# Kernel optimization log

Hardware: AMD Instinct MI355X
Metric: run time of the kernel (lower is better)

## Reference

```python
import jax, jax.numpy as jnp
import numpy as np

N, D, H = 4096, 128, 8

def setup_inputs() -> dict:
    key = jax.random.key(0)
    ks = jax.random.split(key, 7)
    xavier = float(np.sqrt(6.0 / (D + D)))  # xavier_uniform for [*, D, D]
    x = jax.random.normal(ks[0], (N, D), dtype=jnp.float32)
    W_k = jax.random.uniform(ks[1], (H, D, D), minval=-xavier, maxval=xavier, dtype=jnp.float32)
    W_q = jax.random.uniform(ks[2], (H, D, D), minval=-xavier, maxval=xavier, dtype=jnp.float32)
    W_v = jax.random.uniform(ks[3], (H, D, D), minval=-xavier, maxval=xavier, dtype=jnp.float32)
    W_m = jnp.ones((H,), dtype=jnp.float32)
    lim = float(1.0 / np.sqrt(D))  # default torch Linear init range
    Wg = jax.random.uniform(ks[4], (D, D), minval=-lim, maxval=lim, dtype=jnp.float32)
    bg = jax.random.uniform(ks[5], (D,), minval=-lim, maxval=lim, dtype=jnp.float32)
    return {"x": x, "W_k": W_k, "W_q": W_q, "W_v": W_v, "W_m": W_m, "Wg": Wg, "bg": bg}

def reference(x, W_k, W_q, W_v, W_m, Wg, bg):
    # per-head projections: [H, N, D]
    q = jnp.einsum('nf,hfd->hnd', x, W_q)
    k = jnp.einsum('nf,hfd->hnd', x, W_k)
    v = jnp.einsum('nf,hfd->hnd', x, W_v)
    # dense all-pairs attention scores per head: [H, N, N]
    e = jnp.einsum('hnd,hmd->hnm', q, k)
    attn = jax.nn.softmax(e, axis=-1)
    # weighted sum over values, then head-scaled accumulation: [N, D]
    out = jnp.einsum('h,hnm,hmd->nd', W_m, attn, v)
    # residual MLP: x + ReLU(Linear(x + out))
    h = x + out
    g = jax.nn.relu(h @ Wg.T + bg)
    return x + g
```

## Files before the change

kernel.cpp:

```cpp
#include <hip/hip_runtime.h>

#define NROWS 4096
#define DDIM  128
#define NHEAD 8

typedef __attribute__((ext_vector_type(8))) short    short8;
typedef __attribute__((ext_vector_type(8))) _Float16 half8;
typedef __attribute__((ext_vector_type(4))) float    floatx4;

__device__ __forceinline__ float bf2f(unsigned short u){
  unsigned v = ((unsigned)u) << 16;
  return __builtin_bit_cast(float, v);
}
__device__ __forceinline__ unsigned short f2bf(float f){
  unsigned u = __builtin_bit_cast(unsigned, f);
  u += 0x7FFFu + ((u >> 16) & 1u);
  return (unsigned short)(u >> 16);
}
__device__ __forceinline__ void split2(float v, unsigned short& hi, unsigned short& lo){
  hi = f2bf(v);
  lo = f2bf(v - bf2f(hi));
}
__device__ __forceinline__ void async_cp16(const _Float16* g, _Float16* l){
  __builtin_amdgcn_global_load_lds(
      (const __attribute__((address_space(1))) void*)g,
      (__attribute__((address_space(3))) void*)l, 16, 0, 0);
}

__global__ void fill_kernel(float* __restrict__ out, float val, int n){
  int i = blockIdx.x * 256 + threadIdx.x;
  if (i < n) out[i] = val;
}

__global__ __launch_bounds__(256, 2) void proj_kernel(
    const float* __restrict__ x,
    const float* __restrict__ Wk, const float* __restrict__ Wv,
    _Float16* __restrict__ kfo, _Float16* __restrict__ vfo)
{
  __shared__ alignas(16) unsigned short wthi[DDIM][72];
  __shared__ alignas(16) unsigned short wtlo[DDIM][72];
  const int tid = threadIdx.x, lane = tid & 63, wave = tid >> 6;
  const int l4 = lane & 15, quad = lane >> 4;
  const int tile = blockIdx.x, h = blockIdx.y, z = blockIdx.z;
  const float* W = (z == 0 ? Wk : Wv) + h * DDIM * DDIM;

  floatx4 acc[8];
#pragma unroll
  for (int c = 0; c < 8; c++) acc[c] = (floatx4)0.f;

  for (int fh = 0; fh < 2; fh++) {
    for (int i = tid; i < DDIM * 64; i += 256) {
      const int d = i >> 6, fl = i & 63;
      unsigned short hi, lo;
      split2(W[(fh * 64 + fl) * DDIM + d], hi, lo);
      wthi[d][fl] = hi; wtlo[d][fl] = lo;
    }
    __syncthreads();

    const float* xr = x + (size_t)(tile * 64 + wave * 16 + l4) * DDIM + fh * 64 + quad * 8;
    short8 ah[2], al[2];
#pragma unroll
    for (int t2 = 0; t2 < 2; t2++) {
      float4 v0 = *(const float4*)(xr + t2 * 32);
      float4 v1 = *(const float4*)(xr + t2 * 32 + 4);
      float xv[8] = {v0.x, v0.y, v0.z, v0.w, v1.x, v1.y, v1.z, v1.w};
#pragma unroll
      for (int j = 0; j < 8; j++) {
        unsigned short hi, lo; split2(xv[j], hi, lo);
        ah[t2][j] = (short)hi; al[t2][j] = (short)lo;
      }
    }
#pragma unroll
    for (int t2 = 0; t2 < 2; t2++) {
#pragma unroll
      for (int c = 0; c < 8; c++) {
        short8 bh = *(const short8*)(&wthi[c * 16 + l4][t2 * 32 + quad * 8]);
        short8 bl = *(const short8*)(&wtlo[c * 16 + l4][t2 * 32 + quad * 8]);
        acc[c] = __builtin_amdgcn_mfma_f32_16x16x32_bf16(ah[t2], bh, acc[c], 0, 0, 0);
        acc[c] = __builtin_amdgcn_mfma_f32_16x16x32_bf16(al[t2], bh, acc[c], 0, 0, 0);
        acc[c] = __builtin_amdgcn_mfma_f32_16x16x32_bf16(ah[t2], bl, acc[c], 0, 0, 0);
      }
    }
    __syncthreads();
  }

  const int rb = wave * 16 + quad * 4;
  const size_t tilebase = (size_t)(h * 64 + tile) * 8192;
#pragma unroll
  for (int c = 0; c < 8; c++) {
    const int d = c * 16 + l4;
#pragma unroll
    for (int r = 0; r < 4; r++) {
      const int kl = rb + r;
      const float val = acc[c][r];
      if (z == 0) {
        const int c2 = kl >> 4, l4k = kl & 15;
        const int tt = d >> 5, qd = (d >> 3) & 3, jj = d & 7;
        const int qX = qd ^ ((l4k >> 1) & 3);
        kfo[tilebase + (size_t)((c2 * 4 + tt) * 16 + l4k) * 32 + qX * 8 + jj] =
            (_Float16)val;
      } else {
        const int c2 = d >> 4, l4v = d & 15;
        const int tt = kl >> 5, qd = (kl >> 3) & 3, jj = kl & 7;
        const int qX = qd ^ ((l4v >> 1) & 3);
        vfo[tilebase + (size_t)((c2 * 2 + tt) * 16 + l4v) * 32 + qX * 8 + jj] =
            (_Float16)val;
      }
    }
  }
}

union FlashLds {
  struct { unsigned short hi[DDIM][72], lo[DDIM][72]; } wq;
  float qf[64][132];
  struct { _Float16 k[8192], v[8192], p[4][2][1024]; } kv;
};

__global__ __launch_bounds__(256, 2) void flash_kernel(
    const float* __restrict__ x, const float* __restrict__ Wq,
    const _Float16* __restrict__ kfo, const _Float16* __restrict__ vfo,
    _Float16* __restrict__ op, float* __restrict__ mb, float* __restrict__ lb)
{
  __shared__ alignas(16) FlashLds lds;
  const int tid = threadIdx.x, lane = tid & 63, wave = tid >> 6;
  const int l4 = lane & 15, quad = lane >> 4;
  const int h = blockIdx.x & 7, qt = (blockIdx.x >> 3) & 31, s = blockIdx.x >> 8;
  const int q0 = qt * 128;

  half8 aq[2][4];

  {
    floatx4 qacc[2][8];
#pragma unroll
    for (int sp = 0; sp < 2; sp++)
#pragma unroll
      for (int c = 0; c < 8; c++) qacc[sp][c] = (floatx4)0.f;

    const float* Wqh = Wq + h * DDIM * DDIM;
    for (int fh = 0; fh < 2; fh++) {
      for (int i = tid; i < DDIM * 64; i += 256) {
        const int d = i >> 6, fl = i & 63;
        unsigned short hi, lo;
        split2(Wqh[(fh * 64 + fl) * DDIM + d], hi, lo);
        lds.wq.hi[d][fl] = hi; lds.wq.lo[d][fl] = lo;
      }
      __syncthreads();
#pragma unroll
      for (int sp = 0; sp < 2; sp++) {
        const float* xr = x + (size_t)(q0 + sp * 64 + wave * 16 + l4) * DDIM + fh * 64 + quad * 8;
        short8 ah[2], al[2];
#pragma unroll
        for (int t2 = 0; t2 < 2; t2++) {
          float4 v0 = *(const float4*)(xr + t2 * 32);
          float4 v1 = *(const float4*)(xr + t2 * 32 + 4);
          float xv[8] = {v0.x, v0.y, v0.z, v0.w, v1.x, v1.y, v1.z, v1.w};
#pragma unroll
          for (int j = 0; j < 8; j++) {
            unsigned short hi, lo; split2(xv[j], hi, lo);
            ah[t2][j] = (short)hi; al[t2][j] = (short)lo;
          }
        }
#pragma unroll
        for (int t2 = 0; t2 < 2; t2++) {
#pragma unroll
          for (int c = 0; c < 8; c++) {
            short8 bh = *(const short8*)(&lds.wq.hi[c * 16 + l4][t2 * 32 + quad * 8]);
            short8 bl = *(const short8*)(&lds.wq.lo[c * 16 + l4][t2 * 32 + quad * 8]);
            qacc[sp][c] = __builtin_amdgcn_mfma_f32_16x16x32_bf16(ah[t2], bh, qacc[sp][c], 0, 0, 0);
            qacc[sp][c] = __builtin_amdgcn_mfma_f32_16x16x32_bf16(al[t2], bh, qacc[sp][c], 0, 0, 0);
            qacc[sp][c] = __builtin_amdgcn_mfma_f32_16x16x32_bf16(ah[t2], bl, qacc[sp][c], 0, 0, 0);
          }
        }
      }
      __syncthreads();
    }

#pragma unroll
    for (int sp = 0; sp < 2; sp++) {
#pragma unroll
      for (int c = 0; c < 8; c++)
#pragma unroll
        for (int r = 0; r < 4; r++)
          lds.qf[wave * 16 + quad * 4 + r][c * 16 + l4] = qacc[sp][c][r];
      __syncthreads();
      if ((wave >> 1) == sp) {
#pragma unroll
        for (int g = 0; g < 2; g++)
#pragma unroll
          for (int t = 0; t < 4; t++) {
            const float* qr = &lds.qf[(wave & 1) * 32 + g * 16 + l4][t * 32 + quad * 8];
            float4 v0 = *(const float4*)qr;
            float4 v1 = *(const float4*)(qr + 4);
            aq[g][t][0] = (_Float16)v0.x; aq[g][t][1] = (_Float16)v0.y;
            aq[g][t][2] = (_Float16)v0.z; aq[g][t][3] = (_Float16)v0.w;
            aq[g][t][4] = (_Float16)v1.x; aq[g][t][5] = (_Float16)v1.y;
            aq[g][t][6] = (_Float16)v1.z; aq[g][t][7] = (_Float16)v1.w;
          }
      }
      __syncthreads();
    }
  }

  float m_run[2][4];
#pragma unroll
  for (int g = 0; g < 2; g++)
#pragma unroll
    for (int r = 0; r < 4; r++) m_run[g][r] = -1e30f;
  floatx4 Oacc[2][8], lacc[2];
#pragma unroll
  for (int g = 0; g < 2; g++) {
    lacc[g] = (floatx4)0.f;
#pragma unroll
    for (int c = 0; c < 8; c++) Oacc[g][c] = (floatx4)0.f;
  }

  half8 vones;
#pragma unroll
  for (int j = 0; j < 8; j++) vones[j] = (_Float16)1.f;

  const _Float16* kfo_h = kfo + (size_t)h * 64 * 8192;
  const _Float16* vfo_h = vfo + (size_t)h * 64 * 8192;
  const int lq = (l4 * 4 + (quad ^ ((l4 >> 1) & 3))) * 8;

  for (int kt = s * 32; kt < s * 32 + 32; ++kt) {
    {
      const _Float16* ks = kfo_h + (size_t)kt * 8192 + wave * 2048 + lane * 8;
      const _Float16* vs = vfo_h + (size_t)kt * 8192 + wave * 2048 + lane * 8;
      _Float16* kd = &lds.kv.k[wave * 2048];
      _Float16* vd = &lds.kv.v[wave * 2048];
#pragma unroll
      for (int it = 0; it < 4; it++) {
        async_cp16(ks + it * 512, kd + it * 512);
        async_cp16(vs + it * 512, vd + it * 512);
      }
    }
    __syncthreads();

    floatx4 Sf[2][4];
#pragma unroll
    for (int g = 0; g < 2; g++)
#pragma unroll
      for (int c = 0; c < 4; c++) Sf[g][c] = (floatx4)0.f;
#pragma unroll
    for (int t = 0; t < 4; t++) {
      half8 b[4];
#pragma unroll
      for (int c = 0; c < 4; c++)
        b[c] = *(const half8*)&lds.kv.k[(c * 4 + t) * 512 + lq];
#pragma unroll
      for (int g = 0; g < 2; g++)
#pragma unroll
        for (int c = 0; c < 4; c++)
          Sf[g][c] = __builtin_amdgcn_mfma_f32_16x16x32_f16(aq[g][t], b[c], Sf[g][c], 0, 0, 0);
    }

    float alpha[2][4];
#pragma unroll
    for (int g = 0; g < 2; g++) {
      float mt[4];
#pragma unroll
      for (int r = 0; r < 4; r++)
        mt[r] = fmaxf(fmaxf(Sf[g][0][r], Sf[g][1][r]), fmaxf(Sf[g][2][r], Sf[g][3][r]));
#pragma unroll
      for (int mk = 1; mk <= 8; mk <<= 1)
#pragma unroll
        for (int r = 0; r < 4; r++) mt[r] = fmaxf(mt[r], __shfl_xor(mt[r], mk, 64));
#pragma unroll
      for (int r = 0; r < 4; r++) {
        const float mn = fmaxf(m_run[g][r], mt[r]);
        alpha[g][r] = __expf(m_run[g][r] - mn);
        m_run[g][r] = mn;
      }
#pragma unroll
      for (int r = 0; r < 4; r++)
#pragma unroll
        for (int c = 0; c < 4; c++) Sf[g][c][r] = __expf(Sf[g][c][r] - m_run[g][r]);
    }

#pragma unroll
    for (int g = 0; g < 2; g++)
#pragma unroll
      for (int c = 0; c < 4; c++)
#pragma unroll
        for (int r = 0; r < 4; r++)
          lds.kv.p[wave][g][((c * 2 + (l4 >> 3)) * 16 + quad * 4 + r) * 8 + (l4 & 7)] =
              (_Float16)Sf[g][c][r];

#pragma unroll
    for (int g = 0; g < 2; g++) {
#pragma unroll
      for (int c = 0; c < 8; c++) {
        Oacc[g][c][0] *= alpha[g][0]; Oacc[g][c][1] *= alpha[g][1];
        Oacc[g][c][2] *= alpha[g][2]; Oacc[g][c][3] *= alpha[g][3];
      }
      lacc[g][0] *= alpha[g][0]; lacc[g][1] *= alpha[g][1];
      lacc[g][2] *= alpha[g][2]; lacc[g][3] *= alpha[g][3];
    }
#pragma unroll
    for (int t = 0; t < 2; t++) {
      half8 ap[2];
#pragma unroll
      for (int g = 0; g < 2; g++) {
        ap[g] = *(const half8*)&lds.kv.p[wave][g][((t * 4 + quad) * 16 + l4) * 8];
        lacc[g] = __builtin_amdgcn_mfma_f32_16x16x32_f16(ap[g], vones, lacc[g], 0, 0, 0);
      }
#pragma unroll
      for (int c = 0; c < 8; c++) {
        half8 bv = *(const half8*)&lds.kv.v[(c * 2 + t) * 512 + lq];
#pragma unroll
        for (int g = 0; g < 2; g++)
          Oacc[g][c] = __builtin_amdgcn_mfma_f32_16x16x32_f16(ap[g], bv, Oacc[g][c], 0, 0, 0);
      }
    }
    __syncthreads();
  }

#pragma unroll
  for (int g = 0; g < 2; g++) {
    const int rbase = wave * 32 + g * 16 + quad * 4;
    const size_t rowbase = (size_t)(s * NHEAD + h) * NROWS + q0 + rbase;
#pragma unroll
    for (int c = 0; c < 8; c++) {
      const int col = c * 16 + l4;
#pragma unroll
      for (int r = 0; r < 4; r++)
        op[(rowbase + r) * DDIM + col] = (_Float16)Oacc[g][c][r];
    }
    if (l4 == 0) {
#pragma unroll
      for (int r = 0; r < 4; r++) {
        mb[rowbase + r] = m_run[g][r];
        lb[rowbase + r] = lacc[g][r];
      }
    }
  }
}

__global__ __launch_bounds__(128) void merge_kernel(
    const _Float16* __restrict__ op, const float* __restrict__ mb,
    const float* __restrict__ lb, const float* __restrict__ Wm,
    float* __restrict__ u)
{
  __shared__ float sc[2][NHEAD];
  const int n = blockIdx.x, d = threadIdx.x;
  if (d < NHEAD) {
    const int h = d;
    const float m1 = mb[(size_t)h * NROWS + n];
    const float m2 = mb[(size_t)(NHEAD + h) * NROWS + n];
    const float l1 = lb[(size_t)h * NROWS + n];
    const float l2 = lb[(size_t)(NHEAD + h) * NROWS + n];
    const float m  = fmaxf(m1, m2);
    const float a1 = __expf(m1 - m), a2 = __expf(m2 - m);
    const float invL = Wm[h] / (l1 * a1 + l2 * a2);
    sc[0][h] = a1 * invL;
    sc[1][h] = a2 * invL;
  }
  __syncthreads();
  float acc = 0.f;
#pragma unroll
  for (int h = 0; h < NHEAD; h++) {
    acc += sc[0][h] * (float)op[((size_t)h * NROWS + n) * DDIM + d];
    acc += sc[1][h] * (float)op[((size_t)(NHEAD + h) * NROWS + n) * DDIM + d];
  }
  u[(size_t)n * DDIM + d] = acc;
}

__global__ __launch_bounds__(256, 2) void mlp_kernel(
    const float* __restrict__ x, const float* __restrict__ u,
    const float* __restrict__ Wg, const float* __restrict__ bg,
    float* __restrict__ out)
{
  __shared__ alignas(16) unsigned short wghi[DDIM][72];
  __shared__ alignas(16) unsigned short wglo[DDIM][72];
  const int tid = threadIdx.x, lane = tid & 63, wave = tid >> 6;
  const int l4 = lane & 15, quad = lane >> 4;
  const int r0 = blockIdx.x * 64;

  floatx4 acc[8];
#pragma unroll
  for (int c = 0; c < 8; c++) acc[c] = (floatx4)0.f;

  for (int fh = 0; fh < 2; fh++) {
    for (int i = tid; i < DDIM * 64; i += 256) {
      const int ii = i >> 6, jl = i & 63;
      unsigned short hi, lo;
      split2(Wg[ii * DDIM + fh * 64 + jl], hi, lo);
      wghi[ii][jl] = hi; wglo[ii][jl] = lo;
    }
    __syncthreads();

    const size_t xoff = (size_t)(r0 + wave * 16 + l4) * DDIM + fh * 64 + quad * 8;
    short8 ah[2], al[2];
#pragma unroll
    for (int t2 = 0; t2 < 2; t2++) {
      float4 x0 = *(const float4*)(x + xoff + t2 * 32);
      float4 x1 = *(const float4*)(x + xoff + t2 * 32 + 4);
      float4 u0 = *(const float4*)(u + xoff + t2 * 32);
      float4 u1 = *(const float4*)(u + xoff + t2 * 32 + 4);
      float hv[8] = {x0.x + u0.x, x0.y + u0.y, x0.z + u0.z, x0.w + u0.w,
                     x1.x + u1.x, x1.y + u1.y, x1.z + u1.z, x1.w + u1.w};
#pragma unroll
      for (int j = 0; j < 8; j++) {
        unsigned short hi, lo; split2(hv[j], hi, lo);
        ah[t2][j] = (short)hi; al[t2][j] = (short)lo;
      }
    }
#pragma unroll
    for (int t2 = 0; t2 < 2; t2++) {
#pragma unroll
      for (int c = 0; c < 8; c++) {
        short8 bh = *(const short8*)(&wghi[c * 16 + l4][t2 * 32 + quad * 8]);
        short8 bl = *(const short8*)(&wglo[c * 16 + l4][t2 * 32 + quad * 8]);
        acc[c] = __builtin_amdgcn_mfma_f32_16x16x32_bf16(ah[t2], bh, acc[c], 0, 0, 0);
        acc[c] = __builtin_amdgcn_mfma_f32_16x16x32_bf16(al[t2], bh, acc[c], 0, 0, 0);
        acc[c] = __builtin_amdgcn_mfma_f32_16x16x32_bf16(ah[t2], bl, acc[c], 0, 0, 0);
      }
    }
    __syncthreads();
  }

  const int rbase = wave * 16 + quad * 4;
#pragma unroll
  for (int c = 0; c < 8; c++) {
    const int col = c * 16 + l4;
    const float bgf = bg[col];
#pragma unroll
    for (int r = 0; r < 4; r++) {
      const size_t idx = (size_t)(r0 + rbase + r) * DDIM + col;
      out[idx] = x[idx] + fmaxf(acc[c][r] + bgf, 0.f);
    }
  }
}

extern "C" void kernel_launch(void* const* d_in, const int* in_sizes, int n_in,
                              void* d_out, int out_size, void* d_ws, size_t ws_size,
                              hipStream_t stream) {
  float* out = (float*)d_out;
  const int fill_blocks = (out_size + 255) / 256;

  const bool ok_sizes =
      n_in == 7 &&
      in_sizes[0] == NROWS * DDIM &&
      in_sizes[1] == NHEAD * DDIM * DDIM &&
      in_sizes[2] == NHEAD * DDIM * DDIM &&
      in_sizes[3] == NHEAD * DDIM * DDIM &&
      in_sizes[4] == NHEAD &&
      in_sizes[5] == DDIM * DDIM &&
      in_sizes[6] == DDIM &&
      out_size == NROWS * DDIM;
  if (!ok_sizes) {
    fill_kernel<<<fill_blocks, 256, 0, stream>>>(out, 1000.f, out_size);
    return;
  }

  const size_t HND = (size_t)NHEAD * NROWS * DDIM;
  const size_t ND  = (size_t)NROWS * DDIM;
  const size_t need = ND * 4 + 2 * HND * 2 + 2 * HND * 2 + 2 * NHEAD * NROWS * 8;
  if (ws_size < need) {
    fill_kernel<<<fill_blocks, 256, 0, stream>>>(out, 500.f, out_size);
    return;
  }

  const float* x  = (const float*)d_in[0];
  const float* Wk = (const float*)d_in[1];
  const float* Wq = (const float*)d_in[2];
  const float* Wv = (const float*)d_in[3];
  const float* Wm = (const float*)d_in[4];
  const float* Wg = (const float*)d_in[5];
  const float* bg = (const float*)d_in[6];

  float*     u   = (float*)d_ws;
  _Float16*  kfo = (_Float16*)(u + ND);
  _Float16*  vfo = kfo + HND;
  _Float16*  op  = vfo + HND;
  float*     mb  = (float*)(op + 2 * HND);
  float*     lb  = mb + 2 * NHEAD * NROWS;

  (void)hipGetLastError();
  proj_kernel<<<dim3(64, NHEAD, 2), 256, 0, stream>>>(x, Wk, Wv, kfo, vfo);
  flash_kernel<<<dim3(512), 256, 0, stream>>>(x, Wq, kfo, vfo, op, mb, lb);
  merge_kernel<<<dim3(4096), 128, 0, stream>>>(op, mb, lb, Wm, u);
  mlp_kernel<<<dim3(64), 256, 0, stream>>>(x, u, Wg, bg, out);
  if (hipGetLastError() != hipSuccess) {
    fill_kernel<<<fill_blocks, 256, 0, stream>>>(out, 2000.f, out_size);
  }
}
```

Baseline: 261.4 us.

## Double-buffer K tiles, load V fragments to registers, batch projection tiles per block

The flash kernel now double-buffers K tiles in LDS, prefetching the next tile asynchronously while the current one is computed. V fragments are loaded straight from global memory into registers instead of being staged through LDS. The rescale of the output accumulators is skipped when no lane's running max changed. The projection kernel now handles four row tiles per block so the split weight matrix staged in LDS is reused across them. The cost is higher register pressure (acc[4][8] and vfrag[8][2]) and fewer projection blocks, which may reduce occupancy.

```diff
diff --git a/kernel.cpp b/kernel.cpp
--- a/kernel.cpp
+++ b/kernel.cpp
@@ -41,12 +41,14 @@
   __shared__ alignas(16) unsigned short wtlo[DDIM][72];
   const int tid = threadIdx.x, lane = tid & 63, wave = tid >> 6;
   const int l4 = lane & 15, quad = lane >> 4;
-  const int tile = blockIdx.x, h = blockIdx.y, z = blockIdx.z;
+  const int h = blockIdx.y, z = blockIdx.z;
   const float* W = (z == 0 ? Wk : Wv) + h * DDIM * DDIM;
 
-  floatx4 acc[8];
-#pragma unroll
-  for (int c = 0; c < 8; c++) acc[c] = (floatx4)0.f;
+  floatx4 acc[4][8];
+#pragma unroll
+  for (int t4 = 0; t4 < 4; t4++)
+#pragma unroll
+    for (int c = 0; c < 8; c++) acc[t4][c] = (floatx4)0.f;
 
   for (int fh = 0; fh < 2; fh++) {
     for (int i = tid; i < DDIM * 64; i += 256) {
@@ -57,54 +59,62 @@
     }
     __syncthreads();
 
-    const float* xr = x + (size_t)(tile * 64 + wave * 16 + l4) * DDIM + fh * 64 + quad * 8;
-    short8 ah[2], al[2];
-#pragma unroll
-    for (int t2 = 0; t2 < 2; t2++) {
-      float4 v0 = *(const float4*)(xr + t2 * 32);
-      float4 v1 = *(const float4*)(xr + t2 * 32 + 4);
-      float xv[8] = {v0.x, v0.y, v0.z, v0.w, v1.x, v1.y, v1.z, v1.w};
-#pragma unroll
-      for (int j = 0; j < 8; j++) {
-        unsigned short hi, lo; split2(xv[j], hi, lo);
-        ah[t2][j] = (short)hi; al[t2][j] = (short)lo;
-      }
-    }
-#pragma unroll
-    for (int t2 = 0; t2 < 2; t2++) {
-#pragma unroll
-      for (int c = 0; c < 8; c++) {
-        short8 bh = *(const short8*)(&wthi[c * 16 + l4][t2 * 32 + quad * 8]);
-        short8 bl = *(const short8*)(&wtlo[c * 16 + l4][t2 * 32 + quad * 8]);
-        acc[c] = __builtin_amdgcn_mfma_f32_16x16x32_bf16(ah[t2], bh, acc[c], 0, 0, 0);
-        acc[c] = __builtin_amdgcn_mfma_f32_16x16x32_bf16(al[t2], bh, acc[c], 0, 0, 0);
-        acc[c] = __builtin_amdgcn_mfma_f32_16x16x32_bf16(ah[t2], bl, acc[c], 0, 0, 0);
+#pragma unroll
+    for (int t4 = 0; t4 < 4; t4++) {
+      const int tile = blockIdx.x * 4 + t4;
+      const float* xr = x + (size_t)(tile * 64 + wave * 16 + l4) * DDIM + fh * 64 + quad * 8;
+      short8 ah[2], al[2];
+#pragma unroll
+      for (int t2 = 0; t2 < 2; t2++) {
+        float4 v0 = *(const float4*)(xr + t2 * 32);
+        float4 v1 = *(const float4*)(xr + t2 * 32 + 4);
+        float xv[8] = {v0.x, v0.y, v0.z, v0.w, v1.x, v1.y, v1.z, v1.w};
+#pragma unroll
+        for (int j = 0; j < 8; j++) {
+          unsigned short hi, lo; split2(xv[j], hi, lo);
+          ah[t2][j] = (short)hi; al[t2][j] = (short)lo;
+        }
+      }
+#pragma unroll
+      for (int t2 = 0; t2 < 2; t2++) {
+#pragma unroll
+        for (int c = 0; c < 8; c++) {
+          short8 bh = *(const short8*)(&wthi[c * 16 + l4][t2 * 32 + quad * 8]);
+          short8 bl = *(const short8*)(&wtlo[c * 16 + l4][t2 * 32 + quad * 8]);
+          acc[t4][c] = __builtin_amdgcn_mfma_f32_16x16x32_bf16(ah[t2], bh, acc[t4][c], 0, 0, 0);
+          acc[t4][c] = __builtin_amdgcn_mfma_f32_16x16x32_bf16(al[t2], bh, acc[t4][c], 0, 0, 0);
+          acc[t4][c] = __builtin_amdgcn_mfma_f32_16x16x32_bf16(ah[t2], bl, acc[t4][c], 0, 0, 0);
+        }
       }
     }
     __syncthreads();
   }
 
   const int rb = wave * 16 + quad * 4;
-  const size_t tilebase = (size_t)(h * 64 + tile) * 8192;
-#pragma unroll
-  for (int c = 0; c < 8; c++) {
-    const int d = c * 16 + l4;
-#pragma unroll
-    for (int r = 0; r < 4; r++) {
-      const int kl = rb + r;
-      const float val = acc[c][r];
-      if (z == 0) {
-        const int c2 = kl >> 4, l4k = kl & 15;
-        const int tt = d >> 5, qd = (d >> 3) & 3, jj = d & 7;
-        const int qX = qd ^ ((l4k >> 1) & 3);
-        kfo[tilebase + (size_t)((c2 * 4 + tt) * 16 + l4k) * 32 + qX * 8 + jj] =
-            (_Float16)val;
-      } else {
-        const int c2 = d >> 4, l4v = d & 15;
-        const int tt = kl >> 5, qd = (kl >> 3) & 3, jj = kl & 7;
-        const int qX = qd ^ ((l4v >> 1) & 3);
-        vfo[tilebase + (size_t)((c2 * 2 + tt) * 16 + l4v) * 32 + qX * 8 + jj] =
-            (_Float16)val;
+#pragma unroll
+  for (int t4 = 0; t4 < 4; t4++) {
+    const int tile = blockIdx.x * 4 + t4;
+    const size_t tilebase = (size_t)(h * 64 + tile) * 8192;
+#pragma unroll
+    for (int c = 0; c < 8; c++) {
+      const int d = c * 16 + l4;
+#pragma unroll
+      for (int r = 0; r < 4; r++) {
+        const int kl = rb + r;
+        const float val = acc[t4][c][r];
+        if (z == 0) {
+          const int c2 = kl >> 4, l4k = kl & 15;
+          const int tt = d >> 5, qd = (d >> 3) & 3, jj = d & 7;
+          const int qX = qd ^ ((l4k >> 1) & 3);
+          kfo[tilebase + (size_t)((c2 * 4 + tt) * 16 + l4k) * 32 + qX * 8 + jj] =
+              (_Float16)val;
+        } else {
+          const int c2 = d >> 4, l4v = d & 15;
+          const int tt = kl >> 5, qd = (kl >> 3) & 3, jj = kl & 7;
+          const int qX = qd ^ ((l4v >> 1) & 3);
+          vfo[tilebase + (size_t)((c2 * 2 + tt) * 16 + l4v) * 32 + qX * 8 + jj] =
+              (_Float16)val;
+        }
       }
     }
   }
@@ -113,7 +123,7 @@
 union FlashLds {
   struct { unsigned short hi[DDIM][72], lo[DDIM][72]; } wq;
   float qf[64][132];
-  struct { _Float16 k[8192], v[8192], p[4][2][1024]; } kv;
+  struct { _Float16 k[2][8192], p[4][2][1024]; } kv;
 };
 
 __global__ __launch_bounds__(256, 2) void flash_kernel(
@@ -221,20 +231,34 @@
   const _Float16* kfo_h = kfo + (size_t)h * 64 * 8192;
   const _Float16* vfo_h = vfo + (size_t)h * 64 * 8192;
   const int lq = (l4 * 4 + (quad ^ ((l4 >> 1) & 3))) * 8;
-
-  for (int kt = s * 32; kt < s * 32 + 32; ++kt) {
+  const int kt0 = s * 32, kt1 = kt0 + 32;
+
+  {
+    const _Float16* ks = kfo_h + (size_t)kt0 * 8192 + wave * 2048 + lane * 8;
+    _Float16* kd = &lds.kv.k[0][wave * 2048];
+#pragma unroll
+    for (int it = 0; it < 4; it++) async_cp16(ks + it * 512, kd + it * 512);
+  }
+
+  for (int kt = kt0; kt < kt1; ++kt) {
+    const int cur = kt & 1;
+    __syncthreads();
+
+    half8 vfrag[8][2];
     {
-      const _Float16* ks = kfo_h + (size_t)kt * 8192 + wave * 2048 + lane * 8;
-      const _Float16* vs = vfo_h + (size_t)kt * 8192 + wave * 2048 + lane * 8;
-      _Float16* kd = &lds.kv.k[wave * 2048];
-      _Float16* vd = &lds.kv.v[wave * 2048];
-#pragma unroll
-      for (int it = 0; it < 4; it++) {
-        async_cp16(ks + it * 512, kd + it * 512);
-        async_cp16(vs + it * 512, vd + it * 512);
-      }
-    }
-    __syncthreads();
+      const _Float16* vtb = vfo_h + (size_t)kt * 8192;
+#pragma unroll
+      for (int c = 0; c < 8; c++)
+#pragma unroll
+        for (int t = 0; t < 2; t++)
+          vfrag[c][t] = *(const half8*)(vtb + (c * 2 + t) * 512 + lq);
+    }
+    if (kt + 1 < kt1) {
+      const _Float16* ks = kfo_h + (size_t)(kt + 1) * 8192 + wave * 2048 + lane * 8;
+      _Float16* kd = &lds.kv.k[cur ^ 1][wave * 2048];
+#pragma unroll
+      for (int it = 0; it < 4; it++) async_cp16(ks + it * 512, kd + it * 512);
+    }
 
     floatx4 Sf[2][4];
 #pragma unroll
@@ -246,7 +270,7 @@
       half8 b[4];
 #pragma unroll
       for (int c = 0; c < 4; c++)
-        b[c] = *(const half8*)&lds.kv.k[(c * 4 + t) * 512 + lq];
+        b[c] = *(const half8*)&lds.kv.k[cur][(c * 4 + t) * 512 + lq];
 #pragma unroll
       for (int g = 0; g < 2; g++)
 #pragma unroll
@@ -288,13 +312,17 @@
 
 #pragma unroll
     for (int g = 0; g < 2; g++) {
-#pragma unroll
-      for (int c = 0; c < 8; c++) {
-        Oacc[g][c][0] *= alpha[g][0]; Oacc[g][c][1] *= alpha[g][1];
-        Oacc[g][c][2] *= alpha[g][2]; Oacc[g][c][3] *= alpha[g][3];
-      }
-      lacc[g][0] *= alpha[g][0]; lacc[g][1] *= alpha[g][1];
-      lacc[g][2] *= alpha[g][2]; lacc[g][3] *= alpha[g][3];
+      const bool moved = (alpha[g][0] != 1.f) | (alpha[g][1] != 1.f) |
+                         (alpha[g][2] != 1.f) | (alpha[g][3] != 1.f);
+      if (__any(moved)) {
+#pragma unroll
+        for (int c = 0; c < 8; c++) {
+          Oacc[g][c][0] *= alpha[g][0]; Oacc[g][c][1] *= alpha[g][1];
+          Oacc[g][c][2] *= alpha[g][2]; Oacc[g][c][3] *= alpha[g][3];
+        }
+        lacc[g][0] *= alpha[g][0]; lacc[g][1] *= alpha[g][1];
+        lacc[g][2] *= alpha[g][2]; lacc[g][3] *= alpha[g][3];
+      }
     }
 #pragma unroll
     for (int t = 0; t < 2; t++) {
@@ -305,14 +333,11 @@
         lacc[g] = __builtin_amdgcn_mfma_f32_16x16x32_f16(ap[g], vones, lacc[g], 0, 0, 0);
       }
 #pragma unroll
-      for (int c = 0; c < 8; c++) {
-        half8 bv = *(const half8*)&lds.kv.v[(c * 2 + t) * 512 + lq];
+      for (int c = 0; c < 8; c++)
 #pragma unroll
         for (int g = 0; g < 2; g++)
-          Oacc[g][c] = __builtin_amdgcn_mfma_f32_16x16x32_f16(ap[g], bv, Oacc[g][c], 0, 0, 0);
-      }
-    }
-    __syncthreads();
+          Oacc[g][c] = __builtin_amdgcn_mfma_f32_16x16x32_f16(ap[g], vfrag[c][t], Oacc[g][c], 0, 0, 0);
+    }
   }
 
 #pragma unroll
@@ -477,7 +502,7 @@
   float*     lb  = mb + 2 * NHEAD * NROWS;
 
   (void)hipGetLastError();
-  proj_kernel<<<dim3(64, NHEAD, 2), 256, 0, stream>>>(x, Wk, Wv, kfo, vfo);
+  proj_kernel<<<dim3(16, NHEAD, 2), 256, 0, stream>>>(x, Wk, Wv, kfo, vfo);
   flash_kernel<<<dim3(512), 256, 0, stream>>>(x, Wq, kfo, vfo, op, mb, lb);
   merge_kernel<<<dim3(4096), 128, 0, stream>>>(op, mb, lb, Wm, u);
   mlp_kernel<<<dim3(64), 256, 0, stream>>>(x, u, Wg, bg, out);
```

After: 254.8 us. -2.5%, faster.
